# Performance work log

Hardware: AMD Instinct MI355X
Metric: run time of the kernel (lower is better)

Reference implementation:

```python
import jax, jax.numpy as jnp
import numpy as np

N = 12000      # nodes
E = 384000     # edges (avg degree 32)
IN, HID, OUT = 128, 128, 40
BETA, ITERS = 0.5, 25   # Bjorck order-2 projection params (module defaults)


def setup_inputs() -> dict:
    key = jax.random.key(0)
    ks = jax.random.split(key, 6)
    x = jax.random.normal(ks[0], (N, IN), jnp.float32)
    edge_index = jax.random.randint(ks[1], (2, E), 0, N, dtype=jnp.int32)
    W1 = jax.random.normal(ks[2], (HID, IN), jnp.float32)
    W2 = jax.random.normal(ks[3], (HID, HID), jnp.float32)
    lin_w = jax.random.normal(ks[4], (OUT, HID), jnp.float32) / np.float32(np.sqrt(HID))
    lin_b = jax.random.normal(ks[5], (OUT,), jnp.float32) * 0.01
    return {"x": x, "W1": W1, "W2": W2, "lin_w": lin_w, "lin_b": lin_b,
            "edge_index": edge_index}


def _bjorck(w):
    # order-2 Bjorck orthonormalization (beta fixed at 0.5):
    # w <- 15/8 w - 5/4 w(w^T w) + 3/8 w(w^T w)^2
    for _ in range(ITERS):
        wtw = w.T @ w
        w = 1.875 * w - 1.25 * (w @ wtw) + 0.375 * (w @ (wtw @ wtw))
    return w


def _orthonormal(W):
    # scale_values: sqrt(||W||_inf * ||W||_1) upper-bounds the spectral norm
    # (computed on .data in torch -> stop_gradient here)
    scaling = jnp.sqrt(jnp.abs(W).sum(axis=1).max() * jnp.abs(W).sum(axis=0).max())
    scaling = jax.lax.stop_gradient(scaling)
    return _bjorck(W.T / scaling).T  # [out, in]


def _normalized_adj(edge_index):
    # to_dense_adj (scatter-add) then D^{-1/2} A^T D^{-1/2} exactly as
    # normalize_tensor_adj: adj.dot(D^{-1/2}).T.dot(D^{-1/2})
    r, c = edge_index[0], edge_index[1]
    adj = jnp.zeros((N, N), jnp.float32).at[r, c].add(1.0)
    rowsum = adj.sum(axis=1)
    d = jnp.where(rowsum > 0, rowsum ** -0.5, 0.0)
    return d[:, None] * adj.T * d[None, :]


def reference(x, W1, W2, lin_w, lin_b, edge_index):
    norm_adj = _normalized_adj(edge_index)          # [N, N]
    h = jax.nn.relu(norm_adj @ (x @ _orthonormal(W1).T))   # [N, HID]
    h = jax.nn.relu(norm_adj @ (h @ _orthonormal(W2).T))   # [N, HID]
    # dropout inactive (eval mode)
    logits = h @ lin_w.T + lin_b                    # [N, OUT]
    return jax.nn.log_softmax(logits, axis=1)
```

## Files before the change

### kernel.cpp

```cpp
#include <hip/hip_runtime.h>
#include <math.h>

#define NN 12000
#define EE 384000
#define FF 128
#define NOUT 40
#define BJ_MAX 25
#define NWARM 8
#define EXIT_TOL 3e-3f
#define GEMM_BLOCKS ((NN + 63) / 64)
#define SEG1 3
#define SEG2 6
#define SEG3 9
#define NDB 32
#define ESL (EE / NDB)
#define ESL4 (ESL / 4)

typedef __attribute__((ext_vector_type(8))) short bf16x8;
typedef __attribute__((ext_vector_type(4))) short s16x4;
typedef __attribute__((ext_vector_type(4))) float f32x4;
typedef unsigned short ushort_t;

__device__ __forceinline__ ushort_t f2bf(float x) {
  unsigned u = __float_as_uint(x);
  unsigned r = (u + 0x7FFFu + ((u >> 16) & 1u)) >> 16;
  return (ushort_t)r;
}
__device__ __forceinline__ float bf2f(ushort_t h) {
  return __uint_as_float(((unsigned)h) << 16);
}
__device__ __forceinline__ int swz(int r, int c) {
  return ((r << 8) + (c << 1)) ^ ((r & 7) << 4);
}

__device__ __forceinline__ void mm_product(const char* Xh, const char* Xl,
    const char* Yh, const char* Yl, int R0, int C0, int lane, f32x4 (&acc)[2][4]) {
  int rl = lane & 15;
  int kq = (lane >> 4) * 8;
  #pragma unroll
  for (int k0 = 0; k0 < 128; k0 += 32) {
    bf16x8 ah[2], al[2];
    #pragma unroll
    for (int i = 0; i < 2; i++) {
      ah[i] = *(const bf16x8*)(Xh + swz(R0 + i * 16 + rl, k0 + kq));
      al[i] = *(const bf16x8*)(Xl + swz(R0 + i * 16 + rl, k0 + kq));
    }
    #pragma unroll
    for (int j = 0; j < 4; j++) {
      bf16x8 bh = *(const bf16x8*)(Yh + swz(C0 + j * 16 + rl, k0 + kq));
      bf16x8 bl = *(const bf16x8*)(Yl + swz(C0 + j * 16 + rl, k0 + kq));
      #pragma unroll
      for (int i = 0; i < 2; i++) {
        acc[i][j] = __builtin_amdgcn_mfma_f32_16x16x32_bf16(ah[i], bh, acc[i][j], 0, 0, 0);
        acc[i][j] = __builtin_amdgcn_mfma_f32_16x16x32_bf16(ah[i], bl, acc[i][j], 0, 0, 0);
        acc[i][j] = __builtin_amdgcn_mfma_f32_16x16x32_bf16(al[i], bh, acc[i][j], 0, 0, 0);
      }
    }
  }
}

__device__ __forceinline__ void store_C(char* Ch, char* Cl, int R0, int C0,
    int lane, f32x4 (&acc)[2][4]) {
  int cl = lane & 15, rq = (lane >> 4) * 4;
  #pragma unroll
  for (int i = 0; i < 2; i++)
  #pragma unroll
  for (int j = 0; j < 4; j++) {
    int col = C0 + j * 16 + cl;
    int row = R0 + i * 16 + rq;
    s16x4 hv, lv;
    #pragma unroll
    for (int t = 0; t < 4; t++) {
      float x = acc[i][j][t];
      ushort_t h = f2bf(x);
      ushort_t lo = f2bf(x - bf2f(h));
      hv[t] = (short)h; lv[t] = (short)lo;
    }
    *(s16x4*)(Ch + swz(col, row)) = hv;
    *(s16x4*)(Cl + swz(col, row)) = lv;
  }
}

__device__ __forceinline__ void store_CR(char* Ch, char* Cl, char* Rh, char* Rl,
    int R0, int C0, int lane, f32x4 (&acc)[2][4]) {
  int cl = lane & 15, rq = (lane >> 4) * 4;
  #pragma unroll
  for (int i = 0; i < 2; i++)
  #pragma unroll
  for (int j = 0; j < 4; j++) {
    int col = C0 + j * 16 + cl;
    int row = R0 + i * 16 + rq;
    s16x4 hv, lv;
    #pragma unroll
    for (int t = 0; t < 4; t++) {
      float x = acc[i][j][t];
      ushort_t h = f2bf(x);
      ushort_t lo = f2bf(x - bf2f(h));
      hv[t] = (short)h; lv[t] = (short)lo;
    }
    *(s16x4*)(Ch + swz(col, row)) = hv;
    *(s16x4*)(Cl + swz(col, row)) = lv;
    #pragma unroll
    for (int t = 0; t < 4; t++) {
      *(ushort_t*)(Rh + swz(row + t, col)) = (ushort_t)(unsigned short)hv[t];
      *(ushort_t*)(Rl + swz(row + t, col)) = (ushort_t)(unsigned short)lv[t];
    }
  }
}

__device__ void bjorck_segment(char* lds, float* wmax, int L, int s_it, int e_it,
    int is_last, const float* __restrict__ W1, const float* __restrict__ W2,
    ushort_t* __restrict__ wfc, char* __restrict__ state) {
  char* P0h = lds;
  char* P0l = lds + 32768;
  char* P1h = lds + 65536;
  char* P1l = lds + 98304;
  const float* Wsrc = (L == 0) ? W1 : W2;
  int tid = threadIdx.x;
  int lane = tid & 63;
  int wv = tid >> 6;
  int R0 = (wv >> 1) * 32;
  int C0 = (wv & 1) * 64;
  char* st = state + L * 131072;

  if (s_it == 0) {
    float* f = (float*)lds;
    if (tid < 256) {
      float s = 0.0f;
      if (tid < 128) {
        for (int j = 0; j < FF; j++) s += fabsf(Wsrc[tid * FF + j]);
      } else {
        int c = tid - 128;
        for (int j = 0; j < FF; j++) s += fabsf(Wsrc[j * FF + c]);
      }
      f[tid] = s;
    }
    __syncthreads();
    if (tid == 0) {
      float rm = 0.0f, cm = 0.0f;
      for (int i = 0; i < 128; i++) { rm = fmaxf(rm, f[i]); cm = fmaxf(cm, f[128 + i]); }
      f[256] = 1.0f / sqrtf(rm * cm);
    }
    __syncthreads();
    float inv_s = f[256];
    __syncthreads();
    int r = tid >> 2, c0 = (tid & 3) * 32;
    #pragma unroll
    for (int mm = 0; mm < 32; mm += 8) {
      bf16x8 hv, lv;
      #pragma unroll
      for (int t = 0; t < 8; t++) {
        float x = Wsrc[r * FF + c0 + mm + t] * inv_s;
        ushort_t h = f2bf(x);
        ushort_t lo = f2bf(x - bf2f(h));
        hv[t] = (short)h; lv[t] = (short)lo;
      }
      *(bf16x8*)(P0h + swz(r, c0 + mm)) = hv;
      *(bf16x8*)(P0l + swz(r, c0 + mm)) = lv;
      #pragma unroll
      for (int t = 0; t < 8; t++) {
        *(ushort_t*)(P1h + swz(c0 + mm + t, r)) = (ushort_t)(unsigned short)hv[t];
        *(ushort_t*)(P1l + swz(c0 + mm + t, r)) = (ushort_t)(unsigned short)lv[t];
      }
    }
    __syncthreads();
  } else {
    int4* dst = (int4*)lds;
    const int4* src = (const int4*)st;
    for (int i = tid; i < 8192; i += 512) dst[i] = src[i];
    __syncthreads();
  }

  int done = 0;
  for (int it = s_it; it < e_it; it++) {
    float ca, cb, cc;
    if (it < NWARM)       { ca = 3.4445f; cb = -4.7750f; cc = 2.0315f; }
    else if (it == NWARM) { ca = 2.1479f; cb = -1.7258f; cc = 0.5645f; }
    else                  { ca = 1.875f;  cb = -1.25f;   cc = 0.375f; }

    f32x4 m_acc[2][4] = {};
    mm_product(P0h, P0l, P0h, P0l, R0, C0, lane, m_acc);

    if (it > NWARM) {
      int cl = lane & 15, rq = (lane >> 4) * 4;
      float lmax = 0.0f;
      #pragma unroll
      for (int i = 0; i < 2; i++)
      #pragma unroll
      for (int j = 0; j < 4; j++)
      #pragma unroll
      for (int t = 0; t < 4; t++) {
        int row = R0 + i * 16 + rq + t;
        int col = C0 + j * 16 + cl;
        float d = m_acc[i][j][t] - ((row == col) ? 1.0f : 0.0f);
        lmax = fmaxf(lmax, fabsf(d));
      }
      #pragma unroll
      for (int off = 32; off; off >>= 1) lmax = fmaxf(lmax, __shfl_xor(lmax, off));
      if (lane == 0) wmax[wv] = lmax;
      __syncthreads();
      float gmax = 0.0f;
      #pragma unroll
      for (int w = 0; w < 8; w++) gmax = fmaxf(gmax, wmax[w]);
      if (gmax < EXIT_TOL) { done = 1; break; }
    } else {
      __syncthreads();
    }
    store_C(P0h, P0l, R0, C0, lane, m_acc);
    __syncthreads();

    f32x4 p_acc[2][4] = {};
    mm_product(P0h, P0l, P0h, P0l, R0, C0, lane, p_acc);
    {
      int cl = lane & 15, rq = (lane >> 4) * 4;
      #pragma unroll
      for (int i = 0; i < 2; i++)
      #pragma unroll
      for (int j = 0; j < 4; j++)
      #pragma unroll
      for (int t = 0; t < 4; t++) {
        int row = R0 + i * 16 + rq + t;
        int col = C0 + j * 16 + cl;
        float pv = cb * m_acc[i][j][t] + cc * p_acc[i][j][t];
        if (row == col) pv += ca;
        p_acc[i][j][t] = pv;
      }
    }
    __syncthreads();
    store_C(P0h, P0l, R0, C0, lane, p_acc);
    __syncthreads();

    f32x4 v_acc[2][4] = {};
    mm_product(P0h, P0l, P1h, P1l, R0, C0, lane, v_acc);
    __syncthreads();
    store_CR(P1h, P1l, P0h, P0l, R0, C0, lane, v_acc);
    __syncthreads();
  }

  if (done || is_last) {
    ushort_t* oh = wfc + L * 32768;
    ushort_t* ol = oh + 16384;
    int r = tid >> 2;
    int q = tid & 3;
    #pragma unroll
    for (int b = 0; b < 4; b++) {
      int c0 = q * 32 + b * 8;
      bf16x8 hv = *(const bf16x8*)(P0h + swz(r, c0));
      bf16x8 lv = *(const bf16x8*)(P0l + swz(r, c0));
      *(bf16x8*)(oh + r * FF + c0) = hv;
      *(bf16x8*)(ol + r * FF + c0) = lv;
    }
  } else {
    const int4* src = (const int4*)lds;
    int4* dst = (int4*)st;
    for (int i = tid; i < 8192; i += 512) dst[i] = src[i];
  }
}

__global__ __launch_bounds__(512) void k1_seg_deg(const int* __restrict__ ei,
    int* __restrict__ pr, int* __restrict__ pc,
    const float* __restrict__ W1, const float* __restrict__ W2,
    ushort_t* __restrict__ wfc, char* __restrict__ state) {
  __shared__ char lds[131072];
  __shared__ float wmax[8];
  if (blockIdx.x >= 2) {
    int b = blockIdx.x - 2;
    int* hist = (int*)lds;
    int tid = threadIdx.x;
    for (int i = tid; i < 24000; i += 512) hist[i] = 0;
    __syncthreads();
    const int4* r4 = (const int4*)ei + b * ESL4;
    const int4* c4 = (const int4*)(ei + EE) + b * ESL4;
    for (int i = tid; i < ESL4; i += 512) {
      int4 rv = r4[i];
      int4 cv = c4[i];
      atomicAdd(&hist[rv.x], 1); atomicAdd(&hist[rv.y], 1);
      atomicAdd(&hist[rv.z], 1); atomicAdd(&hist[rv.w], 1);
      atomicAdd(&hist[12000 + cv.x], 1); atomicAdd(&hist[12000 + cv.y], 1);
      atomicAdd(&hist[12000 + cv.z], 1); atomicAdd(&hist[12000 + cv.w], 1);
    }
    __syncthreads();
    int* prb = pr + b * 12000;
    int* pcb = pc + b * 12000;
    for (int i = tid; i < 12000; i += 512) {
      prb[i] = hist[i];
      pcb[i] = hist[12000 + i];
    }
    return;
  }
  bjorck_segment(lds, wmax, blockIdx.x, 0, SEG1, 0, W1, W2, wfc, state);
}

__global__ __launch_bounds__(512) void k2_seg_scan(const int* __restrict__ pr,
    const int* __restrict__ pc, int* __restrict__ rowstart, float* __restrict__ dinv,
    int* __restrict__ pcsum,
    const float* __restrict__ W1, const float* __restrict__ W2,
    ushort_t* __restrict__ wfc, char* __restrict__ state) {
  __shared__ char lds[131072];
  __shared__ float wmax[8];
  int tid = threadIdx.x;
  if (blockIdx.x == 2) {
    int* tot = (int*)lds;
    int* sums = tot + 12000;
    for (int i = tid; i < 12000; i += 512) {
      int v = 0;
      #pragma unroll
      for (int b = 0; b < NDB; b++) v += pc[b * 12000 + i];
      tot[i] = v;
    }
    __syncthreads();
    const int CH = 24;
    int base = tid * CH;
    int s = 0;
    int local[CH];
    #pragma unroll
    for (int m = 0; m < CH; m++) {
      int idx = base + m;
      int v = (idx < NN) ? tot[idx] : 0;
      local[m] = s;
      s += v;
    }
    sums[tid] = s;
    __syncthreads();
    for (int off = 1; off < 512; off <<= 1) {
      int v = (tid >= off) ? sums[tid - off] : 0;
      __syncthreads();
      sums[tid] += v;
      __syncthreads();
    }
    int excl = (tid > 0) ? sums[tid - 1] : 0;
    #pragma unroll
    for (int m = 0; m < CH; m++) {
      int idx = base + m;
      if (idx < NN) rowstart[idx] = excl + local[m];
    }
    if (tid == 511) rowstart[NN] = sums[511];
    return;
  }
  if (blockIdx.x == 3) {
    for (int i = tid; i < NN; i += 512) {
      int dv = 0;
      #pragma unroll
      for (int b = 0; b < NDB; b++) dv += pr[b * 12000 + i];
      dinv[i] = (dv > 0) ? (1.0f / sqrtf((float)dv)) : 0.0f;
    }
    return;
  }
  if (blockIdx.x >= 4) {
    int i0 = (blockIdx.x - 4) * 6000;
    for (int i = i0 + tid; i < i0 + 6000; i += 512) {
      int run = 0;
      #pragma unroll
      for (int b = 0; b < NDB; b++) {
        int v = pc[b * 12000 + i];
        pcsum[b * 12000 + i] = run;
        run += v;
      }
    }
    return;
  }
  bjorck_segment(lds, wmax, blockIdx.x, SEG1, SEG2, 0, W1, W2, wfc, state);
}

__global__ __launch_bounds__(512) void k3_seg_scatter(const int* __restrict__ ei,
    const int* __restrict__ rowstart, const int* __restrict__ pcsum,
    int* __restrict__ srcl,
    const float* __restrict__ W1, const float* __restrict__ W2,
    ushort_t* __restrict__ wfc, char* __restrict__ state) {
  __shared__ char lds[131072];
  __shared__ float wmax[8];
  if (blockIdx.x >= 2) {
    int b = blockIdx.x - 2;
    int* co = (int*)lds;
    int* fillL = co + 12000;
    int tid = threadIdx.x;
    const int* ps = pcsum + b * 12000;
    for (int i = tid; i < 12000; i += 512) {
      co[i] = rowstart[i] + ps[i];
      fillL[i] = 0;
    }
    __syncthreads();
    const int4* r4 = (const int4*)ei + b * ESL4;
    const int4* c4 = (const int4*)(ei + EE) + b * ESL4;
    for (int i = tid; i < ESL4; i += 512) {
      int4 cv = c4[i];
      int4 rv = r4[i];
      srcl[co[cv.x] + atomicAdd(&fillL[cv.x], 1)] = rv.x;
      srcl[co[cv.y] + atomicAdd(&fillL[cv.y], 1)] = rv.y;
      srcl[co[cv.z] + atomicAdd(&fillL[cv.z], 1)] = rv.z;
      srcl[co[cv.w] + atomicAdd(&fillL[cv.w], 1)] = rv.w;
    }
    return;
  }
  bjorck_segment(lds, wmax, blockIdx.x, SEG2, SEG3, 0, W1, W2, wfc, state);
}

__global__ __launch_bounds__(512) void k4_seg_spmm(const float* __restrict__ X,
    float* __restrict__ Sout, const float* __restrict__ dinv,
    const int* __restrict__ rowstart, const int* __restrict__ srcl,
    const float* __restrict__ W1, const float* __restrict__ W2,
    ushort_t* __restrict__ wfc, char* __restrict__ state) {
  __shared__ char lds[131072];
  __shared__ float wmax[8];
  if (blockIdx.x >= 2) {
    int g = threadIdx.x >> 5, lane32 = threadIdx.x & 31;
    int row = (blockIdx.x - 2) * 16 + g;
    int s = rowstart[row], e = rowstart[row + 1];
    const float4* G4 = (const float4*)X;
    float4 a0 = make_float4(0.f, 0.f, 0.f, 0.f);
    float4 a1 = make_float4(0.f, 0.f, 0.f, 0.f);
    int p = s;
    for (; p + 2 <= e; p += 2) {
      int r0 = srcl[p], r1 = srcl[p + 1];
      float d0 = dinv[r0], d1 = dinv[r1];
      float4 g0 = G4[r0 * 32 + lane32];
      float4 g1 = G4[r1 * 32 + lane32];
      a0.x += d0 * g0.x; a0.y += d0 * g0.y; a0.z += d0 * g0.z; a0.w += d0 * g0.w;
      a1.x += d1 * g1.x; a1.y += d1 * g1.y; a1.z += d1 * g1.z; a1.w += d1 * g1.w;
    }
    if (p < e) {
      int r0 = srcl[p];
      float d0 = dinv[r0];
      float4 g0 = G4[r0 * 32 + lane32];
      a0.x += d0 * g0.x; a0.y += d0 * g0.y; a0.z += d0 * g0.z; a0.w += d0 * g0.w;
    }
    float dc = dinv[row];
    float4 o;
    o.x = dc * (a0.x + a1.x); o.y = dc * (a0.y + a1.y);
    o.z = dc * (a0.z + a1.z); o.w = dc * (a0.w + a1.w);
    ((float4*)Sout)[row * 32 + lane32] = o;
    return;
  }
  bjorck_segment(lds, wmax, blockIdx.x, SEG3, BJ_MAX, 1, W1, W2, wfc, state);
}

__global__ __launch_bounds__(256) void gemm_mfma(const float* __restrict__ X,
    const ushort_t* __restrict__ wc, float* __restrict__ Out, int do_relu) {
  __shared__ char xlds[32768];
  char* Xh = xlds;
  char* Xl = xlds + 16384;
  int tid = threadIdx.x;
  int row0 = blockIdx.x * 64;

  {
    int r = tid >> 2;
    int q = (tid & 3) * 32;
    int gr = row0 + r;
    #pragma unroll
    for (int b = 0; b < 32; b += 8) {
      bf16x8 hv, lv;
      if (gr < NN) {
        const float4* xp4 = (const float4*)(X + gr * FF + q + b);
        float4 v0 = xp4[0];
        float4 v1 = xp4[1];
        float xv[8] = {v0.x, v0.y, v0.z, v0.w, v1.x, v1.y, v1.z, v1.w};
        #pragma unroll
        for (int t = 0; t < 8; t++) {
          ushort_t h = f2bf(xv[t]);
          hv[t] = (short)h;
          lv[t] = (short)f2bf(xv[t] - bf2f(h));
        }
      } else {
        #pragma unroll
        for (int t = 0; t < 8; t++) { hv[t] = 0; lv[t] = 0; }
      }
      *(bf16x8*)(Xh + swz(r, q + b)) = hv;
      *(bf16x8*)(Xl + swz(r, q + b)) = lv;
    }
  }
  __syncthreads();

  int lane = tid & 63, wv = tid >> 6;
  int R0 = (wv & 1) * 32;
  int C0 = (wv >> 1) * 64;
  int rl = lane & 15, kq = (lane >> 4) * 8;
  f32x4 acc[2][4] = {};
  #pragma unroll
  for (int k0 = 0; k0 < 128; k0 += 32) {
    bf16x8 ah[2], al[2];
    #pragma unroll
    for (int i = 0; i < 2; i++) {
      ah[i] = *(const bf16x8*)(Xh + swz(R0 + i * 16 + rl, k0 + kq));
      al[i] = *(const bf16x8*)(Xl + swz(R0 + i * 16 + rl, k0 + kq));
    }
    #pragma unroll
    for (int j = 0; j < 4; j++) {
      const ushort_t* bp = wc + (C0 + j * 16 + rl) * FF + k0 + kq;
      bf16x8 bh = *(const bf16x8*)bp;
      bf16x8 bl = *(const bf16x8*)(bp + 16384);
      #pragma unroll
      for (int i = 0; i < 2; i++) {
        acc[i][j] = __builtin_amdgcn_mfma_f32_16x16x32_bf16(ah[i], bh, acc[i][j], 0, 0, 0);
        acc[i][j] = __builtin_amdgcn_mfma_f32_16x16x32_bf16(ah[i], bl, acc[i][j], 0, 0, 0);
        acc[i][j] = __builtin_amdgcn_mfma_f32_16x16x32_bf16(al[i], bh, acc[i][j], 0, 0, 0);
      }
    }
  }
  int rq = (lane >> 4) * 4;
  #pragma unroll
  for (int i = 0; i < 2; i++)
  #pragma unroll
  for (int j = 0; j < 4; j++) {
    int col = C0 + j * 16 + rl;
    #pragma unroll
    for (int t = 0; t < 4; t++) {
      int node = row0 + R0 + i * 16 + rq + t;
      float v = acc[i][j][t];
      if (do_relu) v = fmaxf(v, 0.0f);
      if (node < NN) Out[node * FF + col] = v;
    }
  }
}

__global__ __launch_bounds__(256) void spmm_head(const float* __restrict__ G,
    const float* __restrict__ dinv, const int* __restrict__ rowstart,
    const int* __restrict__ srcl, const float* __restrict__ lw,
    const float* __restrict__ lb, float* __restrict__ out) {
  __shared__ float slw[NOUT * 130];
  __shared__ float slb[64];
  __shared__ float sh[8][128];
  int tid = threadIdx.x;
  for (int i = tid; i < NOUT * 32; i += 256) {
    int r = i >> 5, c4 = i & 31;
    float4 v = ((const float4*)lw)[r * 32 + c4];
    float* dst = slw + r * 130 + c4 * 4;
    dst[0] = v.x; dst[1] = v.y; dst[2] = v.z; dst[3] = v.w;
  }
  if (tid < 64) slb[tid] = (tid < NOUT) ? lb[tid] : 0.0f;

  {
    int g = tid >> 5, lane32 = tid & 31;
    int row = blockIdx.x * 8 + g;
    int s = rowstart[row], e = rowstart[row + 1];
    const float4* G4 = (const float4*)G;
    float4 a0 = make_float4(0.f, 0.f, 0.f, 0.f);
    float4 a1 = make_float4(0.f, 0.f, 0.f, 0.f);
    int p = s;
    for (; p + 2 <= e; p += 2) {
      int r0 = srcl[p], r1 = srcl[p + 1];
      float d0 = dinv[r0], d1 = dinv[r1];
      float4 g0 = G4[r0 * 32 + lane32];
      float4 g1 = G4[r1 * 32 + lane32];
      a0.x += d0 * g0.x; a0.y += d0 * g0.y; a0.z += d0 * g0.z; a0.w += d0 * g0.w;
      a1.x += d1 * g1.x; a1.y += d1 * g1.y; a1.z += d1 * g1.z; a1.w += d1 * g1.w;
    }
    if (p < e) {
      int r0 = srcl[p];
      float d0 = dinv[r0];
      float4 g0 = G4[r0 * 32 + lane32];
      a0.x += d0 * g0.x; a0.y += d0 * g0.y; a0.z += d0 * g0.z; a0.w += d0 * g0.w;
    }
    float dc = dinv[row];
    float4 o;
    o.x = fmaxf(dc * (a0.x + a1.x), 0.f); o.y = fmaxf(dc * (a0.y + a1.y), 0.f);
    o.z = fmaxf(dc * (a0.z + a1.z), 0.f); o.w = fmaxf(dc * (a0.w + a1.w), 0.f);
    ((float4*)&sh[g][0])[lane32] = o;
  }
  __syncthreads();

  int lane = tid & 63, w = tid >> 6;
  int ll = (lane < NOUT) ? lane : 0;
  const float2* wrow = (const float2*)(slw + ll * 130);
  #pragma unroll
  for (int rr = 0; rr < 2; rr++) {
    int lrow = w * 2 + rr;
    int node = blockIdx.x * 8 + lrow;
    const float2* hrow = (const float2*)&sh[lrow][0];
    float val = slb[lane];
    #pragma unroll 4
    for (int k = 0; k < 64; k++) {
      float2 w2 = wrow[k];
      float2 h2 = hrow[k];
      val += w2.x * h2.x + w2.y * h2.y;
    }
    float m = (lane < NOUT) ? val : -INFINITY;
    for (int off = 32; off; off >>= 1) m = fmaxf(m, __shfl_down(m, off));
    m = __shfl(m, 0);
    float ex = (lane < NOUT) ? expf(val - m) : 0.0f;
    float ssum = ex;
    for (int off = 32; off; off >>= 1) ssum += __shfl_down(ssum, off);
    ssum = __shfl(ssum, 0);
    if (lane < NOUT) out[node * NOUT + lane] = val - m - logf(ssum);
  }
}

extern "C" void kernel_launch(void* const* d_in, const int* in_sizes, int n_in,
                              void* d_out, int out_size, void* d_ws, size_t ws_size,
                              hipStream_t stream) {
  const float* x  = (const float*)d_in[0];
  const float* W1 = (const float*)d_in[1];
  const float* W2 = (const float*)d_in[2];
  const float* lw = (const float*)d_in[3];
  const float* lb = (const float*)d_in[4];
  const int*   ei = (const int*)d_in[5];
  float* out = (float*)d_out;

  float* base = (float*)d_ws;
  float* wf   = base;
  float* dinv = wf + 32768;
  int* rowstart = (int*)(dinv + NN);
  int* srcl     = rowstart + 12004;
  float* bufA = (float*)(srcl + EE);
  float* bufB = bufA + NN * FF;
  char* state = (char*)(bufB + NN * FF);
  int* pr    = (int*)bufB;
  int* pc    = pr + NDB * 12000;
  int* pcsum = (int*)bufA;
  ushort_t* wfc = (ushort_t*)wf;

  k1_seg_deg<<<2 + NDB, 512, 0, stream>>>(ei, pr, pc, W1, W2, wfc, state);
  k2_seg_scan<<<6, 512, 0, stream>>>(pr, pc, rowstart, dinv, pcsum, W1, W2, wfc, state);
  k3_seg_scatter<<<2 + NDB, 512, 0, stream>>>(ei, rowstart, pcsum, srcl, W1, W2, wfc, state);
  k4_seg_spmm<<<2 + NN / 16, 512, 0, stream>>>(x, bufA, dinv, rowstart, srcl, W1, W2, wfc, state);

  gemm_mfma<<<GEMM_BLOCKS, 256, 0, stream>>>(bufA, wfc, bufB, 1);
  gemm_mfma<<<GEMM_BLOCKS, 256, 0, stream>>>(bufB, wfc + 32768, bufA, 0);
  spmm_head<<<NN / 8, 256, 0, stream>>>(bufA, dinv, rowstart, srcl, lw, lb, out);
}
```

Measured before the change: 265.2 us.

## Fuse two dense GEMMs into one kernel and split degree histogram by type

The two back-to-back MFMA GEMMs (ReLU after the first) are merged into one kernel. The intermediate tile is converted to bf16 hi/lo pairs and kept in LDS, so the full intermediate matrix never round-trips through global memory and one launch is removed. The degree-histogram blocks are also split so each block counts only rows or only columns, doubling block count and halving the LDS histogram per block. The cost is 64KB of LDS per GEMM block, which may lower occupancy.

```diff
diff --git a/kernel.cpp b/kernel.cpp
--- a/kernel.cpp
+++ b/kernel.cpp
@@ -265,27 +265,21 @@
   __shared__ float wmax[8];
   if (blockIdx.x >= 2) {
     int b = blockIdx.x - 2;
+    int type = b >> 5;
+    int sl = b & 31;
     int* hist = (int*)lds;
     int tid = threadIdx.x;
-    for (int i = tid; i < 24000; i += 512) hist[i] = 0;
-    __syncthreads();
-    const int4* r4 = (const int4*)ei + b * ESL4;
-    const int4* c4 = (const int4*)(ei + EE) + b * ESL4;
+    for (int i = tid; i < 12000; i += 512) hist[i] = 0;
+    __syncthreads();
+    const int4* e4 = (const int4*)(ei + (type ? 0 : EE)) + sl * ESL4;
     for (int i = tid; i < ESL4; i += 512) {
-      int4 rv = r4[i];
-      int4 cv = c4[i];
-      atomicAdd(&hist[rv.x], 1); atomicAdd(&hist[rv.y], 1);
-      atomicAdd(&hist[rv.z], 1); atomicAdd(&hist[rv.w], 1);
-      atomicAdd(&hist[12000 + cv.x], 1); atomicAdd(&hist[12000 + cv.y], 1);
-      atomicAdd(&hist[12000 + cv.z], 1); atomicAdd(&hist[12000 + cv.w], 1);
-    }
-    __syncthreads();
-    int* prb = pr + b * 12000;
-    int* pcb = pc + b * 12000;
-    for (int i = tid; i < 12000; i += 512) {
-      prb[i] = hist[i];
-      pcb[i] = hist[12000 + i];
-    }
+      int4 v = e4[i];
+      atomicAdd(&hist[v.x], 1); atomicAdd(&hist[v.y], 1);
+      atomicAdd(&hist[v.z], 1); atomicAdd(&hist[v.w], 1);
+    }
+    __syncthreads();
+    int* dst = (type ? pr : pc) + sl * 12000;
+    for (int i = tid; i < 12000; i += 512) dst[i] = hist[i];
     return;
   }
   bjorck_segment(lds, wmax, blockIdx.x, 0, SEG1, 0, W1, W2, wfc, state);
@@ -434,11 +428,14 @@
   bjorck_segment(lds, wmax, blockIdx.x, SEG3, BJ_MAX, 1, W1, W2, wfc, state);
 }
 
-__global__ __launch_bounds__(256) void gemm_mfma(const float* __restrict__ X,
-    const ushort_t* __restrict__ wc, float* __restrict__ Out, int do_relu) {
-  __shared__ char xlds[32768];
-  char* Xh = xlds;
-  char* Xl = xlds + 16384;
+__global__ __launch_bounds__(256) void gemm_fused(const float* __restrict__ S,
+    const ushort_t* __restrict__ wc1, const ushort_t* __restrict__ wc2,
+    float* __restrict__ Out) {
+  __shared__ char xlds[65536];
+  char* Sh = xlds;
+  char* Sl = xlds + 16384;
+  char* Hh = xlds + 32768;
+  char* Hl = xlds + 49152;
   int tid = threadIdx.x;
   int row0 = blockIdx.x * 64;
 
@@ -450,7 +447,7 @@
     for (int b = 0; b < 32; b += 8) {
       bf16x8 hv, lv;
       if (gr < NN) {
-        const float4* xp4 = (const float4*)(X + gr * FF + q + b);
+        const float4* xp4 = (const float4*)(S + gr * FF + q + b);
         float4 v0 = xp4[0];
         float4 v1 = xp4[1];
         float xv[8] = {v0.x, v0.y, v0.z, v0.w, v1.x, v1.y, v1.z, v1.w};
@@ -464,8 +461,8 @@
         #pragma unroll
         for (int t = 0; t < 8; t++) { hv[t] = 0; lv[t] = 0; }
       }
-      *(bf16x8*)(Xh + swz(r, q + b)) = hv;
-      *(bf16x8*)(Xl + swz(r, q + b)) = lv;
+      *(bf16x8*)(Sh + swz(r, q + b)) = hv;
+      *(bf16x8*)(Sl + swz(r, q + b)) = lv;
     }
   }
   __syncthreads();
@@ -474,40 +471,83 @@
   int R0 = (wv & 1) * 32;
   int C0 = (wv >> 1) * 64;
   int rl = lane & 15, kq = (lane >> 4) * 8;
-  f32x4 acc[2][4] = {};
-  #pragma unroll
-  for (int k0 = 0; k0 < 128; k0 += 32) {
-    bf16x8 ah[2], al[2];
-    #pragma unroll
-    for (int i = 0; i < 2; i++) {
-      ah[i] = *(const bf16x8*)(Xh + swz(R0 + i * 16 + rl, k0 + kq));
-      al[i] = *(const bf16x8*)(Xl + swz(R0 + i * 16 + rl, k0 + kq));
-    }
+
+  {
+    f32x4 acc[2][4] = {};
+    #pragma unroll
+    for (int k0 = 0; k0 < 128; k0 += 32) {
+      bf16x8 ah[2], al[2];
+      #pragma unroll
+      for (int i = 0; i < 2; i++) {
+        ah[i] = *(const bf16x8*)(Sh + swz(R0 + i * 16 + rl, k0 + kq));
+        al[i] = *(const bf16x8*)(Sl + swz(R0 + i * 16 + rl, k0 + kq));
+      }
+      #pragma unroll
+      for (int j = 0; j < 4; j++) {
+        const ushort_t* bp = wc1 + (C0 + j * 16 + rl) * FF + k0 + kq;
+        bf16x8 bh = *(const bf16x8*)bp;
+        bf16x8 bl = *(const bf16x8*)(bp + 16384);
+        #pragma unroll
+        for (int i = 0; i < 2; i++) {
+          acc[i][j] = __builtin_amdgcn_mfma_f32_16x16x32_bf16(ah[i], bh, acc[i][j], 0, 0, 0);
+          acc[i][j] = __builtin_amdgcn_mfma_f32_16x16x32_bf16(ah[i], bl, acc[i][j], 0, 0, 0);
+          acc[i][j] = __builtin_amdgcn_mfma_f32_16x16x32_bf16(al[i], bh, acc[i][j], 0, 0, 0);
+        }
+      }
+    }
+    int rq = (lane >> 4) * 4;
+    #pragma unroll
+    for (int i = 0; i < 2; i++)
     #pragma unroll
     for (int j = 0; j < 4; j++) {
-      const ushort_t* bp = wc + (C0 + j * 16 + rl) * FF + k0 + kq;
-      bf16x8 bh = *(const bf16x8*)bp;
-      bf16x8 bl = *(const bf16x8*)(bp + 16384);
+      int c = C0 + j * 16 + rl;
+      #pragma unroll
+      for (int t = 0; t < 4; t++) {
+        int r = R0 + i * 16 + rq + t;
+        float x = fmaxf(acc[i][j][t], 0.0f);
+        ushort_t h = f2bf(x);
+        ushort_t lo = f2bf(x - bf2f(h));
+        *(ushort_t*)(Hh + swz(r, c)) = h;
+        *(ushort_t*)(Hl + swz(r, c)) = lo;
+      }
+    }
+  }
+  __syncthreads();
+
+  {
+    f32x4 acc[2][4] = {};
+    #pragma unroll
+    for (int k0 = 0; k0 < 128; k0 += 32) {
+      bf16x8 ah[2], al[2];
       #pragma unroll
       for (int i = 0; i < 2; i++) {
-        acc[i][j] = __builtin_amdgcn_mfma_f32_16x16x32_bf16(ah[i], bh, acc[i][j], 0, 0, 0);
-        acc[i][j] = __builtin_amdgcn_mfma_f32_16x16x32_bf16(ah[i], bl, acc[i][j], 0, 0, 0);
-        acc[i][j] = __builtin_amdgcn_mfma_f32_16x16x32_bf16(al[i], bh, acc[i][j], 0, 0, 0);
-      }
-    }
-  }
-  int rq = (lane >> 4) * 4;
-  #pragma unroll
-  for (int i = 0; i < 2; i++)
-  #pragma unroll
-  for (int j = 0; j < 4; j++) {
-    int col = C0 + j * 16 + rl;
-    #pragma unroll
-    for (int t = 0; t < 4; t++) {
-      int node = row0 + R0 + i * 16 + rq + t;
-      float v = acc[i][j][t];
-      if (do_relu) v = fmaxf(v, 0.0f);
-      if (node < NN) Out[node * FF + col] = v;
+        ah[i] = *(const bf16x8*)(Hh + swz(R0 + i * 16 + rl, k0 + kq));
+        al[i] = *(const bf16x8*)(Hl + swz(R0 + i * 16 + rl, k0 + kq));
+      }
+      #pragma unroll
+      for (int j = 0; j < 4; j++) {
+        const ushort_t* bp = wc2 + (C0 + j * 16 + rl) * FF + k0 + kq;
+        bf16x8 bh = *(const bf16x8*)bp;
+        bf16x8 bl = *(const bf16x8*)(bp + 16384);
+        #pragma unroll
+        for (int i = 0; i < 2; i++) {
+          acc[i][j] = __builtin_amdgcn_mfma_f32_16x16x32_bf16(ah[i], bh, acc[i][j], 0, 0, 0);
+          acc[i][j] = __builtin_amdgcn_mfma_f32_16x16x32_bf16(ah[i], bl, acc[i][j], 0, 0, 0);
+          acc[i][j] = __builtin_amdgcn_mfma_f32_16x16x32_bf16(al[i], bh, acc[i][j], 0, 0, 0);
+        }
+      }
+    }
+    int rq = (lane >> 4) * 4;
+    #pragma unroll
+    for (int i = 0; i < 2; i++)
+    #pragma unroll
+    for (int j = 0; j < 4; j++) {
+      int col = C0 + j * 16 + rl;
+      #pragma unroll
+      for (int t = 0; t < 4; t++) {
+        int node = row0 + R0 + i * 16 + rq + t;
+        if (node < NN) Out[node * FF + col] = acc[i][j][t];
+      }
     }
   }
 }
@@ -608,12 +648,11 @@
   int* pcsum = (int*)bufA;
   ushort_t* wfc = (ushort_t*)wf;
 
-  k1_seg_deg<<<2 + NDB, 512, 0, stream>>>(ei, pr, pc, W1, W2, wfc, state);
+  k1_seg_deg<<<2 + 2 * NDB, 512, 0, stream>>>(ei, pr, pc, W1, W2, wfc, state);
   k2_seg_scan<<<6, 512, 0, stream>>>(pr, pc, rowstart, dinv, pcsum, W1, W2, wfc, state);
   k3_seg_scatter<<<2 + NDB, 512, 0, stream>>>(ei, rowstart, pcsum, srcl, W1, W2, wfc, state);
   k4_seg_spmm<<<2 + NN / 16, 512, 0, stream>>>(x, bufA, dinv, rowstart, srcl, W1, W2, wfc, state);
 
-  gemm_mfma<<<GEMM_BLOCKS, 256, 0, stream>>>(bufA, wfc, bufB, 1);
-  gemm_mfma<<<GEMM_BLOCKS, 256, 0, stream>>>(bufB, wfc + 32768, bufA, 0);
-  spmm_head<<<NN / 8, 256, 0, stream>>>(bufA, dinv, rowstart, srcl, lw, lb, out);
-}
+  gemm_fused<<<GEMM_BLOCKS, 256, 0, stream>>>(bufA, wfc, wfc + 32768, bufB);
+  spmm_head<<<NN / 8, 256, 0, stream>>>(bufB, dinv, rowstart, srcl, lw, lb, out);
+}
```

Measured after the change: 262.3 us. No clear change (-1.1%).
